# Kernel optimization log

Hardware: AMD Instinct MI355X
Metric: run time of the kernel (lower is better)

Reference implementation:

```python
import jax, jax.numpy as jnp
import numpy as np

B, N, C, H = 2, 2048, 1024, 16
D = C // H  # head dim
SCALE = D ** -0.5


def setup_inputs() -> dict:
    key = jax.random.key(0)
    k1, k2, k3 = jax.random.split(key, 3)
    x = jax.random.normal(k1, (B, N, C), dtype=jnp.float32)
    w_qkv = jax.random.normal(k2, (C, 3 * C), dtype=jnp.float32) * (C ** -0.5)
    w_proj = jax.random.normal(k3, (C, C), dtype=jnp.float32) * (C ** -0.5)
    b_proj = jnp.zeros((C,), dtype=jnp.float32)
    return {"x": x, "w_qkv": w_qkv, "w_proj": w_proj, "b_proj": b_proj}


def reference(x, w_qkv, w_proj, b_proj):
    # qkv projection: [B,N,3C] -> [3,B,H,N,D]
    qkv = (x @ w_qkv).reshape(B, N, 3, H, D).transpose(2, 0, 3, 1, 4)
    q, k, v = qkv[0], qkv[1], qkv[2]
    # attention scores [B,H,N,N]
    attn = jnp.einsum("bhnd,bhmd->bhnm", q, k) * SCALE
    attn = jax.nn.softmax(attn, axis=-1)
    # weighted values -> [B,N,C]
    out = jnp.einsum("bhnm,bhmd->bhnd", attn, v)
    out = out.transpose(0, 2, 1, 3).reshape(B, N, C)
    return out @ w_proj + b_proj
```

## Files before the change

kernel.cpp:

```cpp
#include <hip/hip_runtime.h>
#include <hip/hip_bf16.h>

#define BDIM 2
#define NSEQ 2048
#define CDIM 1024
#define HNUM 16
#define DDIM 64
#define QSCALE 0.18033688f

typedef __attribute__((ext_vector_type(4))) float f4;
typedef __attribute__((ext_vector_type(8))) short s8;

__device__ __forceinline__ unsigned short f2bf_hi(float f) {
  unsigned int u = __float_as_uint(f);
  u += 0x7fffu + ((u >> 16) & 1u);
  return (unsigned short)(u >> 16);
}
__device__ __forceinline__ unsigned int pack_bf16x2(float lo, float hi) {
  __hip_bfloat162 b2 = __float22bfloat162_rn(float2{lo, hi});
  union { __hip_bfloat162 b; unsigned int u; } c;
  c.b = b2;
  return c.u;
}
__device__ __forceinline__ float exp2_raw(float x) {
  float r;
  asm("v_exp_f32 %0, %1" : "=v"(r) : "v"(x));
  return r;
}
__device__ __forceinline__ void gll16(const void* g, void* l) {
  __builtin_amdgcn_global_load_lds(
      (const __attribute__((address_space(1))) unsigned int*)g,
      (__attribute__((address_space(3))) unsigned int*)l, 16, 0, 0);
}

__global__ __launch_bounds__(256)
void prep(const float* __restrict__ X, const float* __restrict__ Wq,
          const float* __restrict__ Wp,
          short* __restrict__ Xh, short* __restrict__ Wqh, short* __restrict__ Wph)
{
  __shared__ float T[64][65];
  const int bx = blockIdx.x;
  const int t = threadIdx.x;

  if (bx < 2048) {
    size_t i = ((size_t)bx * 256 + t) * 8;
    f4 a = *(const f4*)(X + i), b = *(const f4*)(X + i + 4);
    s8 h;
    #pragma unroll
    for (int j = 0; j < 4; ++j) h[j] = (short)f2bf_hi(a[j]);
    #pragma unroll
    for (int j = 0; j < 4; ++j) h[4 + j] = (short)f2bf_hi(b[j]);
    *(s8*)(Xh + i) = h;
    return;
  }

  const float* W;
  short* Th;
  int N, c0, k0;
  if (bx < 2816) {
    int b2 = bx - 2048;
    W = Wq; Th = Wqh; N = 3072;
    c0 = (b2 % 48) * 64; k0 = (b2 / 48) * 64;
  } else {
    int b2 = bx - 2816;
    W = Wp; Th = Wph; N = 1024;
    c0 = (b2 & 15) * 64; k0 = (b2 >> 4) * 64;
  }
  {
    const int r = t >> 2, c16 = (t & 3) * 16;
    const float* src = W + (size_t)(k0 + r) * N + c0 + c16;
    #pragma unroll
    for (int q = 0; q < 4; ++q) {
      f4 v = *(const f4*)(src + q * 4);
      #pragma unroll
      for (int j = 0; j < 4; ++j) T[c16 + q * 4 + j][r] = v[j];
    }
  }
  __syncthreads();
  {
    const int rr = t >> 2, k16 = (t & 3) * 16;
    s8 h0, h1;
    #pragma unroll
    for (int j = 0; j < 8; ++j) h0[j] = (short)f2bf_hi(T[rr][k16 + j]);
    #pragma unroll
    for (int j = 0; j < 8; ++j) h1[j] = (short)f2bf_hi(T[rr][k16 + 8 + j]);
    size_t o = (size_t)(c0 + rr) * 1024 + k0 + k16;
    *(s8*)(Th + o) = h0;
    *(s8*)(Th + o + 8) = h1;
  }
}

__global__ __launch_bounds__(256, 3)
void gemm_qkv(const short* __restrict__ Ah_g, const short* __restrict__ Bth,
              short* __restrict__ Qh, short* __restrict__ Kh, short* __restrict__ Vt)
{
  __shared__ __align__(16) short lds[2][2][128 * 32];
  const int t = threadIdx.x, w = t >> 6, lane = t & 63;
  const int fr = lane & 15, g = lane >> 4;
  const int wr = (w >> 1) * 64, wc = (w & 1) * 64;
  const int m0 = blockIdx.y * 128, c0 = blockIdx.x * 128;

  f4 acc[4][4];
  #pragma unroll
  for (int i = 0; i < 4; ++i)
    #pragma unroll
    for (int j = 0; j < 4; ++j)
      #pragma unroll
      for (int r = 0; r < 4; ++r) acc[i][j][r] = 0.f;

  auto stage = [&](int buf, int kt) {
    const int k0 = kt * 32;
    #pragma unroll
    for (int p = 0; p < 4; ++p) {
      const int plane = p >> 1;
      const int cid = (p & 1) * 256 + t;
      const int r = cid >> 2, c = cid & 3;
      const short* gsrc = (plane == 0)
          ? Ah_g + (size_t)(m0 + r) * 1024 + k0 + c * 8
          : Bth + (size_t)(c0 + r) * 1024 + k0 + c * 8;
      gll16(gsrc, &lds[buf][plane][(p & 1) * 2048 + w * 512]);
    }
  };

  auto compute = [&](int buf) {
    const short* A_h = lds[buf][0];
    const short* B_h = lds[buf][1];
    s8 ah[4], bh[4];
    #pragma unroll
    for (int i = 0; i < 4; ++i) ah[i] = *(const s8*)&A_h[(wr + i * 16 + fr) * 32 + g * 8];
    #pragma unroll
    for (int j = 0; j < 4; ++j) bh[j] = *(const s8*)&B_h[(wc + j * 16 + fr) * 32 + g * 8];
    #pragma unroll
    for (int i = 0; i < 4; ++i)
      #pragma unroll
      for (int j = 0; j < 4; ++j)
        acc[i][j] = __builtin_amdgcn_mfma_f32_16x16x32_bf16(ah[i], bh[j], acc[i][j], 0, 0, 0);
  };

  stage(0, 0);
  __syncthreads();
  int cur = 0;
  for (int kt = 0; kt < 32; ++kt) {
    if (kt + 1 < 32) stage(cur ^ 1, kt + 1);
    compute(cur);
    __syncthreads();
    cur ^= 1;
  }

  const int ts = c0 >> 10;
  const int rbase = g * 4;
  if (ts == 2) {
    #pragma unroll
    for (int i = 0; i < 4; ++i)
      #pragma unroll
      for (int j = 0; j < 4; ++j) {
        int grow = m0 + wr + i * 16 + rbase;
        int gcol = c0 + wc + j * 16 + fr;
        int b = grow >> 11, n = grow & 2047;
        int rem = gcol & 1023, hh = rem >> 6, d = rem & 63;
        short4 pv;
        pv.x = (short)f2bf_hi(acc[i][j][0]);
        pv.y = (short)f2bf_hi(acc[i][j][1]);
        pv.z = (short)f2bf_hi(acc[i][j][2]);
        pv.w = (short)f2bf_hi(acc[i][j][3]);
        *(short4*)(Vt + (((size_t)(b * 16 + hh)) * 64 + d) * 2048 + n) = pv;
      }
  } else {
    #pragma unroll
    for (int i = 0; i < 4; ++i)
      #pragma unroll
      for (int j = 0; j < 4; ++j)
        #pragma unroll
        for (int rr = 0; rr < 4; ++rr) {
          int grow = m0 + wr + i * 16 + rbase + rr;
          int gcol = c0 + wc + j * 16 + fr;
          int b = grow >> 11, n = grow & 2047;
          int rem = gcol & 1023, hh = rem >> 6, d = rem & 63;
          size_t o = (((size_t)(b * 16 + hh)) * 2048 + n) * 64 + d;
          float v = acc[i][j][rr];
          if (ts == 0) Qh[o] = (short)f2bf_hi(v * QSCALE);
          else         Kh[o] = (short)f2bf_hi(v);
        }
  }
}

__global__ __launch_bounds__(256, 2)
void attn(const short* __restrict__ Qh, const short* __restrict__ Kh,
          const short* __restrict__ Vt,
          short* __restrict__ AOh)
{
  __shared__ __align__(16) short kb[2][64 * 64], vb[2][64 * 64];
  __shared__ __align__(16) short pb[4][32][88];
  const int t = threadIdx.x, w = t >> 6, lane = t & 63;
  const int fr = lane & 15, g = lane >> 4;
  const int bid = blockIdx.x;
  const int swz = (bid & 7) * 64 + (bid >> 3);
  const int bh = swz >> 4, qb = swz & 15, q0 = qb * 128;
  const size_t base = (size_t)bh * 2048 * 64;

  s8 qf[2][2];
  #pragma unroll
  for (int qs = 0; qs < 2; ++qs) {
    const int qrow = q0 + w * 32 + qs * 16 + fr;
    #pragma unroll
    for (int ks = 0; ks < 2; ++ks)
      qf[qs][ks] = *(const s8*)(Qh + base + (size_t)qrow * 64 + ks * 32 + g * 8);
  }

  s8 onesf;
  #pragma unroll
  for (int i = 0; i < 8; ++i) onesf[i] = (short)0x3F80;

  f4 oacc[2][4], lacc[2];
  #pragma unroll
  for (int qs = 0; qs < 2; ++qs) {
    #pragma unroll
    for (int dj = 0; dj < 4; ++dj)
      #pragma unroll
      for (int r = 0; r < 4; ++r) oacc[qs][dj][r] = 0.f;
    #pragma unroll
    for (int r = 0; r < 4; ++r) lacc[qs][r] = 0.f;
  }

  auto stage = [&](int buf, int kt) {
    const int kv0 = kt * 64;
    #pragma unroll
    for (int p = 0; p < 2; ++p) {
      const int cid = p * 256 + t;
      const int r = cid >> 3, csw = cid & 7, cl = csw ^ (r & 7);
      gll16(Kh + base + (size_t)(kv0 + r) * 64 + cl * 8, &kb[buf][cid * 8]);
      gll16(Vt + base + (size_t)r * 2048 + kv0 + cl * 8, &vb[buf][cid * 8]);
    }
  };

  auto body = [&](const short* kbuf, const short* vbuf) {
    f4 st[4][2];
    #pragma unroll
    for (int j = 0; j < 4; ++j)
      #pragma unroll
      for (int qs = 0; qs < 2; ++qs)
        #pragma unroll
        for (int r = 0; r < 4; ++r) st[j][qs][r] = 0.f;
    __builtin_amdgcn_s_setprio(1);
    #pragma unroll
    for (int j = 0; j < 4; ++j) {
      const int R = j * 16 + fr;
      #pragma unroll
      for (int ks = 0; ks < 2; ++ks) {
        const int co = ((ks * 4 + g) ^ (R & 7)) * 8;
        s8 khf = *(const s8*)&kbuf[R * 64 + co];
        st[j][0] = __builtin_amdgcn_mfma_f32_16x16x32_bf16(khf, qf[0][ks], st[j][0], 0, 0, 0);
        st[j][1] = __builtin_amdgcn_mfma_f32_16x16x32_bf16(khf, qf[1][ks], st[j][1], 0, 0, 0);
      }
    }
    __builtin_amdgcn_s_setprio(0);

    #pragma unroll
    for (int qs = 0; qs < 2; ++qs)
      #pragma unroll
      for (int j = 0; j < 4; ++j) {
        float p0 = exp2_raw(st[j][qs][0]);
        float p1 = exp2_raw(st[j][qs][1]);
        float p2 = exp2_raw(st[j][qs][2]);
        float p3 = exp2_raw(st[j][qs][3]);
        uint2 wv;
        wv.x = pack_bf16x2(p0, p1);
        wv.y = pack_bf16x2(p2, p3);
        *(uint2*)&pb[w][qs * 16 + fr][j * 16 + g * 4] = wv;
      }

    __builtin_amdgcn_s_setprio(1);
    #pragma unroll
    for (int ks = 0; ks < 2; ++ks) {
      s8 pa0 = *(const s8*)&pb[w][0 * 16 + fr][ks * 32 + g * 8];
      s8 pa1 = *(const s8*)&pb[w][1 * 16 + fr][ks * 32 + g * 8];
      #pragma unroll
      for (int dj = 0; dj < 4; ++dj) {
        const int R = dj * 16 + fr;
        const int co = ((ks * 4 + g) ^ (R & 7)) * 8;
        s8 vbf = *(const s8*)&vbuf[R * 64 + co];
        oacc[0][dj] = __builtin_amdgcn_mfma_f32_16x16x32_bf16(pa0, vbf, oacc[0][dj], 0, 0, 0);
        oacc[1][dj] = __builtin_amdgcn_mfma_f32_16x16x32_bf16(pa1, vbf, oacc[1][dj], 0, 0, 0);
      }
      lacc[0] = __builtin_amdgcn_mfma_f32_16x16x32_bf16(pa0, onesf, lacc[0], 0, 0, 0);
      lacc[1] = __builtin_amdgcn_mfma_f32_16x16x32_bf16(pa1, onesf, lacc[1], 0, 0, 0);
    }
    __builtin_amdgcn_s_setprio(0);
  };

  stage(0, 0);
  for (int kt = 0; kt < 32; kt += 2) {
    __syncthreads();
    stage(1, kt + 1);
    body(kb[0], vb[0]);
    __syncthreads();
    if (kt + 2 < 32) stage(0, kt + 2);
    body(kb[1], vb[1]);
  }

  const int b = bh >> 4, h = bh & 15;
  #pragma unroll
  for (int qs = 0; qs < 2; ++qs) {
    float linv[4];
    #pragma unroll
    for (int r = 0; r < 4; ++r) linv[r] = 1.f / lacc[qs][r];
    #pragma unroll
    for (int dj = 0; dj < 4; ++dj)
      #pragma unroll
      for (int rr = 0; rr < 4; ++rr) {
        int n = q0 + w * 32 + qs * 16 + g * 4 + rr;
        int col = h * 64 + dj * 16 + fr;
        size_t o = ((size_t)b * 2048 + n) * 1024 + col;
        AOh[o] = (short)f2bf_hi(oacc[qs][dj][rr] * linv[rr]);
      }
  }
}

__global__ __launch_bounds__(256, 2)
void gemm_proj(const short* __restrict__ Ah_g, const short* __restrict__ Bth,
               const float* __restrict__ bias, float* __restrict__ OUT)
{
  __shared__ __align__(16) short la[2][4096], lb[2][2048];
  const int t = threadIdx.x, w = t >> 6, lane = t & 63;
  const int fr = lane & 15, g = lane >> 4;
  const int wr = (w >> 1) * 64, wc = (w & 1) * 32;
  const int m0 = blockIdx.y * 128, c0 = blockIdx.x * 64;

  f4 acc[4][2];
  #pragma unroll
  for (int i = 0; i < 4; ++i)
    #pragma unroll
    for (int j = 0; j < 2; ++j)
      #pragma unroll
      for (int r = 0; r < 4; ++r) acc[i][j][r] = 0.f;

  auto stage = [&](int buf, int kt) {
    const int k0 = kt * 32;
    #pragma unroll
    for (int p = 0; p < 2; ++p) {
      const int cid = p * 256 + t;
      const int r = cid >> 2, c = cid & 3;
      gll16(Ah_g + (size_t)(m0 + r) * 1024 + k0 + c * 8, la[buf] + cid * 8);
    }
    {
      const int r = t >> 2, c = t & 3;
      gll16(Bth + (size_t)(c0 + r) * 1024 + k0 + c * 8, lb[buf] + t * 8);
    }
  };

  auto compute = [&](int buf) {
    s8 ah[4], bhf[2];
    #pragma unroll
    for (int i = 0; i < 4; ++i) ah[i] = *(const s8*)&la[buf][(wr + i * 16 + fr) * 32 + g * 8];
    #pragma unroll
    for (int j = 0; j < 2; ++j) bhf[j] = *(const s8*)&lb[buf][(wc + j * 16 + fr) * 32 + g * 8];
    #pragma unroll
    for (int i = 0; i < 4; ++i)
      #pragma unroll
      for (int j = 0; j < 2; ++j)
        acc[i][j] = __builtin_amdgcn_mfma_f32_16x16x32_bf16(ah[i], bhf[j], acc[i][j], 0, 0, 0);
  };

  stage(0, 0);
  __syncthreads();
  int cur = 0;
  for (int kt = 0; kt < 32; ++kt) {
    if (kt + 1 < 32) stage(cur ^ 1, kt + 1);
    compute(cur);
    __syncthreads();
    cur ^= 1;
  }

  const int rbase = g * 4;
  #pragma unroll
  for (int i = 0; i < 4; ++i)
    #pragma unroll
    for (int j = 0; j < 2; ++j)
      #pragma unroll
      for (int rr = 0; rr < 4; ++rr) {
        int grow = m0 + wr + i * 16 + rbase + rr;
        int gcol = c0 + wc + j * 16 + fr;
        OUT[(size_t)grow * 1024 + gcol] = acc[i][j][rr] + bias[gcol];
      }
}

extern "C" void kernel_launch(void* const* d_in, const int* in_sizes, int n_in,
                              void* d_out, int out_size, void* d_ws, size_t ws_size,
                              hipStream_t stream) {
  const float* x      = (const float*)d_in[0];
  const float* w_qkv  = (const float*)d_in[1];
  const float* w_proj = (const float*)d_in[2];
  const float* b_proj = (const float*)d_in[3];
  short* ws = (short*)d_ws;

  const size_t SW = (size_t)3072 * 1024;
  const size_t SP = (size_t)1024 * 1024;
  const size_t SX = (size_t)4096 * 1024;
  short* Wqh = ws;
  short* Wph = Wqh + SW;
  short* Xh  = Wph + SP;
  short* Qh  = Xh + SX;
  short* Kh  = Qh + SX;
  short* Vt  = Kh + SX;
  short* AOh = Xh;

  prep<<<3072, 256, 0, stream>>>(x, w_qkv, w_proj, Xh, Wqh, Wph);
  gemm_qkv<<<dim3(24, 32), 256, 0, stream>>>(Xh, Wqh, Qh, Kh, Vt);
  attn<<<512, 256, 0, stream>>>(Qh, Kh, Vt, AOh);
  gemm_proj<<<dim3(16, 32), 256, 0, stream>>>(AOh, Wph, b_proj, (float*)d_out);
}
```

Measured before the change: 118.8 us.

## Split attention KV range across two warp groups with LDS reduction

Doubles the attention block to 512 threads. Each group of four waves handles half of the key/value sequence, working on 32-row KV tiles with new LDS swizzles. The partial output and row-sum accumulators are then combined through shared memory before normalization. The aim is more waves in flight per block, to hide latency and shorten each wave's serial KV loop. The cost is extra syncs, a reduction epilogue, and possible occupancy limits from the larger block.

```diff
diff --git a/kernel.cpp b/kernel.cpp
--- a/kernel.cpp
+++ b/kernel.cpp
@@ -184,15 +184,17 @@
   }
 }
 
-__global__ __launch_bounds__(256, 2)
+__global__ __launch_bounds__(512, 2)
 void attn(const short* __restrict__ Qh, const short* __restrict__ Kh,
           const short* __restrict__ Vt,
           short* __restrict__ AOh)
 {
-  __shared__ __align__(16) short kb[2][64 * 64], vb[2][64 * 64];
-  __shared__ __align__(16) short pb[4][32][88];
+  __shared__ __align__(16) short kb[2][2][32][64];
+  __shared__ __align__(16) short vb[2][2][64][32];
+  __shared__ __align__(16) short pb[8][32][40];
   const int t = threadIdx.x, w = t >> 6, lane = t & 63;
   const int fr = lane & 15, g = lane >> 4;
+  const int qw = w & 3, hf = w >> 2;
   const int bid = blockIdx.x;
   const int swz = (bid & 7) * 64 + (bid >> 3);
   const int bh = swz >> 4, qb = swz & 15, q0 = qb * 128;
@@ -201,7 +203,7 @@
   s8 qf[2][2];
   #pragma unroll
   for (int qs = 0; qs < 2; ++qs) {
-    const int qrow = q0 + w * 32 + qs * 16 + fr;
+    const int qrow = q0 + qw * 32 + qs * 16 + fr;
     #pragma unroll
     for (int ks = 0; ks < 2; ++ks)
       qf[qs][ks] = *(const s8*)(Qh + base + (size_t)qrow * 64 + ks * 32 + g * 8);
@@ -222,28 +224,33 @@
     for (int r = 0; r < 4; ++r) lacc[qs][r] = 0.f;
   }
 
-  auto stage = [&](int buf, int kt) {
-    const int kv0 = kt * 64;
-    #pragma unroll
-    for (int p = 0; p < 2; ++p) {
-      const int cid = p * 256 + t;
-      const int r = cid >> 3, csw = cid & 7, cl = csw ^ (r & 7);
-      gll16(Kh + base + (size_t)(kv0 + r) * 64 + cl * 8, &kb[buf][cid * 8]);
-      gll16(Vt + base + (size_t)r * 2048 + kv0 + cl * 8, &vb[buf][cid * 8]);
+  auto stage = [&](int buf, int s) {
+    const int c = t;
+    {
+      const int hh = c >> 8, r = (c >> 3) & 31, c8 = c & 7;
+      const int cl = c8 ^ (r & 7);
+      gll16(Kh + base + (size_t)(s * 32 + hh * 1024 + r) * 64 + cl * 8,
+            (short*)kb + buf * 4096 + c * 8);
+    }
+    {
+      const int hh = c >> 8, d = (c >> 2) & 63, c4 = c & 3;
+      const int cv = c4 ^ (d & 3);
+      gll16(Vt + base + (size_t)d * 2048 + s * 32 + hh * 1024 + cv * 8,
+            (short*)vb + buf * 4096 + c * 8);
     }
   };
 
   auto body = [&](const short* kbuf, const short* vbuf) {
-    f4 st[4][2];
-    #pragma unroll
-    for (int j = 0; j < 4; ++j)
+    f4 st[2][2];
+    #pragma unroll
+    for (int j = 0; j < 2; ++j)
       #pragma unroll
       for (int qs = 0; qs < 2; ++qs)
         #pragma unroll
         for (int r = 0; r < 4; ++r) st[j][qs][r] = 0.f;
     __builtin_amdgcn_s_setprio(1);
     #pragma unroll
-    for (int j = 0; j < 4; ++j) {
+    for (int j = 0; j < 2; ++j) {
       const int R = j * 16 + fr;
       #pragma unroll
       for (int ks = 0; ks < 2; ++ks) {
@@ -258,7 +265,7 @@
     #pragma unroll
     for (int qs = 0; qs < 2; ++qs)
       #pragma unroll
-      for (int j = 0; j < 4; ++j) {
+      for (int j = 0; j < 2; ++j) {
         float p0 = exp2_raw(st[j][qs][0]);
         float p1 = exp2_raw(st[j][qs][1]);
         float p2 = exp2_raw(st[j][qs][2]);
@@ -270,49 +277,68 @@
       }
 
     __builtin_amdgcn_s_setprio(1);
-    #pragma unroll
-    for (int ks = 0; ks < 2; ++ks) {
-      s8 pa0 = *(const s8*)&pb[w][0 * 16 + fr][ks * 32 + g * 8];
-      s8 pa1 = *(const s8*)&pb[w][1 * 16 + fr][ks * 32 + g * 8];
-      #pragma unroll
-      for (int dj = 0; dj < 4; ++dj) {
-        const int R = dj * 16 + fr;
-        const int co = ((ks * 4 + g) ^ (R & 7)) * 8;
-        s8 vbf = *(const s8*)&vbuf[R * 64 + co];
-        oacc[0][dj] = __builtin_amdgcn_mfma_f32_16x16x32_bf16(pa0, vbf, oacc[0][dj], 0, 0, 0);
-        oacc[1][dj] = __builtin_amdgcn_mfma_f32_16x16x32_bf16(pa1, vbf, oacc[1][dj], 0, 0, 0);
-      }
-      lacc[0] = __builtin_amdgcn_mfma_f32_16x16x32_bf16(pa0, onesf, lacc[0], 0, 0, 0);
-      lacc[1] = __builtin_amdgcn_mfma_f32_16x16x32_bf16(pa1, onesf, lacc[1], 0, 0, 0);
-    }
+    s8 pa0 = *(const s8*)&pb[w][0 * 16 + fr][g * 8];
+    s8 pa1 = *(const s8*)&pb[w][1 * 16 + fr][g * 8];
+    #pragma unroll
+    for (int dj = 0; dj < 4; ++dj) {
+      const int R = dj * 16 + fr;
+      const int co = (g ^ (R & 3)) * 8;
+      s8 vbf = *(const s8*)&vbuf[R * 32 + co];
+      oacc[0][dj] = __builtin_amdgcn_mfma_f32_16x16x32_bf16(pa0, vbf, oacc[0][dj], 0, 0, 0);
+      oacc[1][dj] = __builtin_amdgcn_mfma_f32_16x16x32_bf16(pa1, vbf, oacc[1][dj], 0, 0, 0);
+    }
+    lacc[0] = __builtin_amdgcn_mfma_f32_16x16x32_bf16(pa0, onesf, lacc[0], 0, 0, 0);
+    lacc[1] = __builtin_amdgcn_mfma_f32_16x16x32_bf16(pa1, onesf, lacc[1], 0, 0, 0);
     __builtin_amdgcn_s_setprio(0);
   };
 
+  const short* kb0 = &kb[0][hf][0][0];
+  const short* vb0 = &vb[0][hf][0][0];
+  const short* kb1 = &kb[1][hf][0][0];
+  const short* vb1 = &vb[1][hf][0][0];
+
   stage(0, 0);
-  for (int kt = 0; kt < 32; kt += 2) {
-    __syncthreads();
-    stage(1, kt + 1);
-    body(kb[0], vb[0]);
-    __syncthreads();
-    if (kt + 2 < 32) stage(0, kt + 2);
-    body(kb[1], vb[1]);
-  }
-
+  for (int s = 0; s < 32; s += 2) {
+    __syncthreads();
+    stage(1, s + 1);
+    body(kb0, vb0);
+    __syncthreads();
+    if (s + 2 < 32) stage(0, s + 2);
+    body(kb1, vb1);
+  }
+
+  __syncthreads();
+  float* pbF = (float*)&pb[0][0][0];
   const int b = bh >> 4, h = bh & 15;
   #pragma unroll
   for (int qs = 0; qs < 2; ++qs) {
-    float linv[4];
-    #pragma unroll
-    for (int r = 0; r < 4; ++r) linv[r] = 1.f / lacc[qs][r];
-    #pragma unroll
-    for (int dj = 0; dj < 4; ++dj)
-      #pragma unroll
-      for (int rr = 0; rr < 4; ++rr) {
-        int n = q0 + w * 32 + qs * 16 + g * 4 + rr;
-        int col = h * 64 + dj * 16 + fr;
-        size_t o = ((size_t)b * 2048 + n) * 1024 + col;
-        AOh[o] = (short)f2bf_hi(oacc[qs][dj][rr] * linv[rr]);
-      }
+    if (hf == 1) {
+      #pragma unroll
+      for (int dj = 0; dj < 4; ++dj)
+        #pragma unroll
+        for (int r = 0; r < 4; ++r)
+          pbF[qw * 1280 + dj * 256 + lane * 4 + r] = oacc[qs][dj][r];
+      #pragma unroll
+      for (int r = 0; r < 4; ++r)
+        pbF[qw * 1280 + 1024 + lane * 4 + r] = lacc[qs][r];
+    }
+    __syncthreads();
+    if (hf == 0) {
+      float linv[4];
+      #pragma unroll
+      for (int r = 0; r < 4; ++r)
+        linv[r] = 1.f / (lacc[qs][r] + pbF[qw * 1280 + 1024 + lane * 4 + r]);
+      #pragma unroll
+      for (int dj = 0; dj < 4; ++dj)
+        #pragma unroll
+        for (int rr = 0; rr < 4; ++rr) {
+          float o = oacc[qs][dj][rr] + pbF[qw * 1280 + dj * 256 + lane * 4 + rr];
+          int n = q0 + qw * 32 + qs * 16 + g * 4 + rr;
+          int col = h * 64 + dj * 16 + fr;
+          AOh[((size_t)b * 2048 + n) * 1024 + col] = (short)f2bf_hi(o * linv[rr]);
+        }
+    }
+    __syncthreads();
   }
 }
 
@@ -406,6 +432,6 @@
 
   prep<<<3072, 256, 0, stream>>>(x, w_qkv, w_proj, Xh, Wqh, Wph);
   gemm_qkv<<<dim3(24, 32), 256, 0, stream>>>(Xh, Wqh, Qh, Kh, Vt);
-  attn<<<512, 256, 0, stream>>>(Qh, Kh, Vt, AOh);
+  attn<<<512, 512, 0, stream>>>(Qh, Kh, Vt, AOh);
   gemm_proj<<<dim3(16, 32), 256, 0, stream>>>(AOh, Wph, b_proj, (float*)d_out);
 }
```

After: 118.0 us. About the same (-0.7%).
